# Kernel optimization log

Hardware: AMD Instinct MI355X
Metric: run time of the kernel (lower is better)

## Reference

```python
import jax, jax.numpy as jnp
import numpy as np

B, D, H, L, P, IMG = 8, 768, 12, 12, 16, 448
GRID = 28  # pos_embed grid (785 = 1 + 28*28)
EPS = 1e-5


def layer_norm(x, g, b):
    mu = jnp.mean(x, axis=-1, keepdims=True)
    var = jnp.mean((x - mu) ** 2, axis=-1, keepdims=True)
    return (x - mu) * jax.lax.rsqrt(var + EPS) * g + b


def setup_inputs() -> dict:
    key = jax.random.key(0)
    ks = jax.random.split(key, 12)
    s = 0.02
    inp = {
        "x": jax.random.normal(ks[0], (B, 3, IMG, IMG), dtype=jnp.float32),
        "conv_w": jax.random.normal(ks[1], (D, 3, P, P), dtype=jnp.float32) * s,
        "conv_b": jnp.zeros((D,), jnp.float32),
        "cls_token": jax.random.normal(ks[2], (1, 1, D), dtype=jnp.float32) * s,
        "pos_embed": jax.random.normal(ks[3], (1, 1 + GRID * GRID, D), dtype=jnp.float32) * s,
        "ln1_g": jnp.ones((L, D), jnp.float32),
        "ln1_b": jnp.zeros((L, D), jnp.float32),
        "qkv_w": jax.random.normal(ks[4], (L, D, 3 * D), dtype=jnp.float32) * s,
        "qkv_b": jnp.zeros((L, 3 * D), jnp.float32),
        "proj_w": jax.random.normal(ks[5], (L, D, D), dtype=jnp.float32) * s,
        "proj_b": jnp.zeros((L, D), jnp.float32),
        "ln2_g": jnp.ones((L, D), jnp.float32),
        "ln2_b": jnp.zeros((L, D), jnp.float32),
        "mlp_w1": jax.random.normal(ks[6], (L, D, 4 * D), dtype=jnp.float32) * s,
        "mlp_b1": jnp.zeros((L, 4 * D), jnp.float32),
        "mlp_w2": jax.random.normal(ks[7], (L, 4 * D, D), dtype=jnp.float32) * s,
        "mlp_b2": jnp.zeros((L, D), jnp.float32),
        "lnf_g": jnp.ones((D,), jnp.float32),
        "lnf_b": jnp.zeros((D,), jnp.float32),
    }
    return inp


def _vit_forward(x, conv_w, conv_b, cls_token, pos_embed,
                 ln1_g, ln1_b, qkv_w, qkv_b, proj_w, proj_b,
                 ln2_g, ln2_b, mlp_w1, mlp_b1, mlp_w2, mlp_b2, lnf_g, lnf_b):
    b = x.shape[0]
    # PatchEmbed: strided conv -> [B, D, 28, 28] -> [B, N, D]
    h = jax.lax.conv_general_dilated(
        x, conv_w, window_strides=(P, P), padding="VALID",
        dimension_numbers=("NCHW", "OIHW", "NCHW")) + conv_b[None, :, None, None]
    gh, gw = h.shape[2], h.shape[3]
    h = h.reshape(b, D, gh * gw).transpose(0, 2, 1)  # [B, N, D]
    # ClassEmbed
    h = jnp.concatenate([jnp.broadcast_to(cls_token, (b, 1, D)), h], axis=1)
    # PosEmbed with bicubic interpolation of the grid part (identity when gh=gw=28)
    grid = pos_embed[:, 1:, :].transpose(0, 2, 1).reshape(1, D, GRID, GRID)
    grid = jax.image.resize(grid, (1, D, gh, gw), method="bicubic")
    grid = grid.reshape(1, D, gh * gw).transpose(0, 2, 1)
    pos = jnp.concatenate([pos_embed[:, :1, :], grid], axis=1)
    h = h + pos

    scale = (D // H) ** (-0.5)

    def block(h, p):
        (l1g, l1b, qw, qb, pw, pb, l2g, l2b, w1, b1, w2, b2) = p
        y = layer_norm(h, l1g, l1b)
        m, n, d = y.shape
        qkv = (y @ qw + qb).reshape(m, n, 3, H, d // H)
        qkv = qkv.transpose(2, 0, 3, 1, 4)  # [3, B, H, N, dh]
        q, k, v = qkv[0], qkv[1], qkv[2]
        w = jax.nn.softmax(jnp.einsum("bhnd,bhmd->bhnm", q, k) * scale, axis=-1)
        attn = jnp.einsum("bhnm,bhmd->bhnd", w, v).transpose(0, 2, 1, 3).reshape(m, n, d)
        h = h + (attn @ pw + pb)
        y = layer_norm(h, l2g, l2b)
        h = h + (jax.nn.gelu(y @ w1 + b1, approximate=False) @ w2 + b2)
        return h, None

    params = (ln1_g, ln1_b, qkv_w, qkv_b, proj_w, proj_b,
              ln2_g, ln2_b, mlp_w1, mlp_b1, mlp_w2, mlp_b2)
    h, _ = jax.lax.scan(block, h, params)
    return layer_norm(h, lnf_g, lnf_b)[:, 0]


def reference(x, conv_w, conv_b, cls_token, pos_embed,
              ln1_g, ln1_b, qkv_w, qkv_b, proj_w, proj_b,
              ln2_g, ln2_b, mlp_w1, mlp_b1, mlp_w2, mlp_b2, lnf_g, lnf_b):
    return _vit_forward(x, conv_w, conv_b, cls_token, pos_embed,
                        ln1_g, ln1_b, qkv_w, qkv_b, proj_w, proj_b,
                        ln2_g, ln2_b, mlp_w1, mlp_b1, mlp_w2, mlp_b2, lnf_g, lnf_b)
```

## Files before the change

kernel.cpp:

```cpp
#include <hip/hip_runtime.h>
#include <math.h>

#define B_   8
#define D_   768
#define H_   12
#define L_   12
#define NTOK 785
#define NPAT 784
#define MTOT (B_ * NTOK)
#define MPAT (B_ * NPAT)
#define MPAD 6400
#define DFF  3072
#define EPS_ 1e-5f

typedef unsigned short u16;
typedef unsigned int   u32;
typedef short s16x8 __attribute__((ext_vector_type(8)));
typedef float f32x4 __attribute__((ext_vector_type(4)));

__device__ __forceinline__ u16 f2b(float f) {
    u32 u = __float_as_uint(f);
    u += 0x7fffu + ((u >> 16) & 1u);
    return (u16)(u >> 16);
}
__device__ __forceinline__ float b2f(u16 s) {
    return __uint_as_float(((u32)s) << 16);
}
__device__ __forceinline__ void gload_lds16(const void* g, void* l) {
    __builtin_amdgcn_global_load_lds(
        (const __attribute__((address_space(1))) void*)g,
        (__attribute__((address_space(3))) void*)l, 16, 0, 0);
}
__device__ __forceinline__ float gelu_exact(float x) {
    return 0.5f * x * (1.0f + erff(x * 0.70710678118654752f));
}

template <int MODE, int OUTBF>
__global__ __launch_bounds__(256) void mfma_gemm(
    const u16* __restrict__ A, const u16* __restrict__ WT,
    const float* __restrict__ bias, const float* __restrict__ R,
    void* __restrict__ Cout, int M, int N, int K)
{
    __shared__ u16 As[128 * 32];
    __shared__ u16 Bs[128 * 32];

    const int bm = blockIdx.y * 128;
    const int bn = blockIdx.x * 128;
    const int t  = threadIdx.x;
    const int wv = t >> 6, ln = t & 63;
    const int wr = wv >> 1, wc = wv & 1;

    f32x4 acc[4][4];
    const f32x4 z4 = {0.f, 0.f, 0.f, 0.f};
#pragma unroll
    for (int i = 0; i < 4; i++)
#pragma unroll
        for (int j = 0; j < 4; j++) acc[i][j] = z4;

    const int lrow = ln & 15;
    const int kq   = (ln >> 4) * 8;

    for (int kt = 0; kt < K; kt += 32) {
        __syncthreads();
#pragma unroll
        for (int g = 0; g < 2; g++) {
            const int c = wv * 64 + g * 256 + ln;
            const int r = c >> 2, kc = (c & 3) * 8;
            u16* ldsA = As + (wv * 64 + g * 256) * 8;
            u16* ldsB = Bs + (wv * 64 + g * 256) * 8;
            gload_lds16(A  + (size_t)(bm + r) * K + kt + kc, ldsA);
            gload_lds16(WT + (size_t)(bn + r) * K + kt + kc, ldsB);
        }
        __syncthreads();

        s16x8 af[4], bf[4];
#pragma unroll
        for (int i = 0; i < 4; i++)
            af[i] = *(const s16x8*)(As + (wr * 64 + i * 16 + lrow) * 32 + kq);
#pragma unroll
        for (int j = 0; j < 4; j++)
            bf[j] = *(const s16x8*)(Bs + (wc * 64 + j * 16 + lrow) * 32 + kq);
#pragma unroll
        for (int i = 0; i < 4; i++)
#pragma unroll
            for (int j = 0; j < 4; j++)
                acc[i][j] = __builtin_amdgcn_mfma_f32_16x16x32_bf16(
                    af[i], bf[j], acc[i][j], 0, 0, 0);
    }

    const int col_l = ln & 15;
    const int rq    = (ln >> 4) * 4;
#pragma unroll
    for (int j = 0; j < 4; j++) {
        const int col = bn + wc * 64 + j * 16 + col_l;
        const float bj = bias[col];
#pragma unroll
        for (int i = 0; i < 4; i++) {
            const int row0 = bm + wr * 64 + i * 16 + rq;
#pragma unroll
            for (int rg = 0; rg < 4; rg++) {
                const int row = row0 + rg;
                if (row >= M) continue;
                float v = acc[i][j][rg] + bj;
                if (MODE == 1) v = gelu_exact(v);
                if (MODE == 2) v += R[(size_t)row * N + col];
                if (OUTBF) ((u16*)Cout)[(size_t)row * N + col] = f2b(v);
                else       ((float*)Cout)[(size_t)row * N + col] = v;
            }
        }
    }
}

__global__ __launch_bounds__(256) void wt_kernel(
    const float* __restrict__ W, u16* __restrict__ WT, int K, int N)
{
    __shared__ float tile[32][33];
    const int n0 = blockIdx.x * 32, k0 = blockIdx.y * 32;
    const int r = threadIdx.x >> 3, c4 = (threadIdx.x & 7) * 4;
    const float4 v = *(const float4*)(W + (size_t)(k0 + r) * N + n0 + c4);
    tile[r][c4 + 0] = v.x; tile[r][c4 + 1] = v.y;
    tile[r][c4 + 2] = v.z; tile[r][c4 + 3] = v.w;
    __syncthreads();
    ushort4 o = make_ushort4(f2b(tile[c4 + 0][r]), f2b(tile[c4 + 1][r]),
                             f2b(tile[c4 + 2][r]), f2b(tile[c4 + 3][r]));
    *(ushort4*)(WT + (size_t)(n0 + r) * K + k0 + c4) = o;
}

__global__ __launch_bounds__(256) void flatcvt_kernel(
    const float* __restrict__ in, u16* __restrict__ out, int n4)
{
    const int i = blockIdx.x * 256 + threadIdx.x;
    if (i >= n4) return;
    const float4 v = ((const float4*)in)[i];
    ((ushort4*)out)[i] = make_ushort4(f2b(v.x), f2b(v.y), f2b(v.z), f2b(v.w));
}

__device__ __forceinline__ float block_sum(float s, float* red) {
#pragma unroll
    for (int off = 32; off; off >>= 1) s += __shfl_down(s, off, 64);
    const int wid = threadIdx.x >> 6;
    if ((threadIdx.x & 63) == 0) red[wid] = s;
    __syncthreads();
    if (threadIdx.x == 0) red[0] = red[0] + red[1] + red[2] + red[3];
    __syncthreads();
    const float r = red[0];
    __syncthreads();
    return r;
}

template <int OUTBF>
__global__ __launch_bounds__(256) void ln_kernel(
    const float* __restrict__ X, const float* __restrict__ g,
    const float* __restrict__ b, void* __restrict__ Y, size_t row_stride_in)
{
    __shared__ float red[4];
    const int row = blockIdx.x;
    const int t = threadIdx.x;
    const float* x = X + (size_t)row * row_stride_in;

    const float v0 = x[t], v1 = x[t + 256], v2 = x[t + 512];
    const float mean = block_sum(v0 + v1 + v2, red) * (1.0f / 768.0f);
    const float d0 = v0 - mean, d1 = v1 - mean, d2 = v2 - mean;
    const float var = block_sum(d0 * d0 + d1 * d1 + d2 * d2, red) * (1.0f / 768.0f);
    const float rs = rsqrtf(var + EPS_);

    const float o0 = d0 * rs * g[t] + b[t];
    const float o1 = d1 * rs * g[t + 256] + b[t + 256];
    const float o2 = d2 * rs * g[t + 512] + b[t + 512];
    if (OUTBF) {
        u16* y = (u16*)Y + (size_t)row * 768;
        y[t] = f2b(o0); y[t + 256] = f2b(o1); y[t + 512] = f2b(o2);
    } else {
        float* y = (float*)Y + (size_t)row * 768;
        y[t] = o0; y[t + 256] = o1; y[t + 512] = o2;
    }
}

#define AQB  128
#define AKT  64
#define KSTR 72

__global__ __launch_bounds__(256) void attn_kernel(
    const u16* __restrict__ qkv, u16* __restrict__ out)
{
    __shared__ u16 Ks[AKT * KSTR];
    __shared__ u16 Vt[64 * KSTR];
    __shared__ u16 Ps[4 * 32 * KSTR];

    const int bh = blockIdx.y;
    const int b  = bh / H_, hh = bh % H_;
    const int q0 = blockIdx.x * AQB;
    const int t  = threadIdx.x;
    const int w  = t >> 6, ln = t & 63;
    const int lrow = ln & 15, quad = ln >> 4;
    const size_t tokbase = (size_t)b * NTOK;

    s16x8 aq[2][2];
#pragma unroll
    for (int rowt = 0; rowt < 2; rowt++) {
        int qr = q0 + w * 32 + rowt * 16 + lrow;
        if (qr > NTOK - 1) qr = NTOK - 1;
        const u16* qp = qkv + (tokbase + qr) * 2304 + hh * 64 + quad * 8;
        aq[rowt][0] = *(const s16x8*)(qp);
        aq[rowt][1] = *(const s16x8*)(qp + 32);
    }

    f32x4 acc_o[2][4];
    const f32x4 z4 = {0.f, 0.f, 0.f, 0.f};
#pragma unroll
    for (int i = 0; i < 2; i++)
#pragma unroll
        for (int j = 0; j < 4; j++) acc_o[i][j] = z4;
    float m_r[2][4], l_r[2][4];
#pragma unroll
    for (int i = 0; i < 2; i++)
#pragma unroll
        for (int j = 0; j < 4; j++) { m_r[i][j] = -1e30f; l_r[i][j] = 0.f; }

    for (int j0 = 0; j0 < NTOK; j0 += AKT) {
        __syncthreads();
#pragma unroll
        for (int g = 0; g < 2; g++) {
            const int c = g * 256 + t;
            const int j = c >> 3, dc = c & 7;
            int jj = j0 + j; if (jj > NTOK - 1) jj = NTOK - 1;
            const s16x8 kv = *(const s16x8*)(
                qkv + (tokbase + jj) * 2304 + 768 + hh * 64 + dc * 8);
            *(s16x8*)(Ks + j * KSTR + dc * 8) = kv;
        }
#pragma unroll
        for (int g = 0; g < 2; g++) {
            const int c = g * 256 + t;
            const int j = c & 63, dc = c >> 6;
            int jj = j0 + j; if (jj > NTOK - 1) jj = NTOK - 1;
            const s16x8 vv = *(const s16x8*)(
                qkv + (tokbase + jj) * 2304 + 1536 + hh * 64 + dc * 8);
#pragma unroll
            for (int e = 0; e < 8; e++)
                Vt[(dc * 8 + e) * KSTR + j] = (u16)((const short*)&vv)[e];
        }
        __syncthreads();

        f32x4 acc_s[2][4];
#pragma unroll
        for (int i = 0; i < 2; i++)
#pragma unroll
            for (int j = 0; j < 4; j++) acc_s[i][j] = z4;
#pragma unroll
        for (int jt = 0; jt < 4; jt++) {
            const s16x8 bk0 =
                *(const s16x8*)(Ks + (jt * 16 + lrow) * KSTR + quad * 8);
            const s16x8 bk1 =
                *(const s16x8*)(Ks + (jt * 16 + lrow) * KSTR + 32 + quad * 8);
#pragma unroll
            for (int rowt = 0; rowt < 2; rowt++) {
                acc_s[rowt][jt] = __builtin_amdgcn_mfma_f32_16x16x32_bf16(
                    aq[rowt][0], bk0, acc_s[rowt][jt], 0, 0, 0);
                acc_s[rowt][jt] = __builtin_amdgcn_mfma_f32_16x16x32_bf16(
                    aq[rowt][1], bk1, acc_s[rowt][jt], 0, 0, 0);
            }
        }
        const f32x4 ninf = {-1e30f, -1e30f, -1e30f, -1e30f};
#pragma unroll
        for (int jt = 0; jt < 4; jt++) {
            const bool valid = (j0 + jt * 16 + lrow) < NTOK;
#pragma unroll
            for (int rowt = 0; rowt < 2; rowt++)
                acc_s[rowt][jt] = valid ? acc_s[rowt][jt] * 0.125f : ninf;
        }

#pragma unroll
        for (int rowt = 0; rowt < 2; rowt++) {
#pragma unroll
            for (int rg = 0; rg < 4; rg++) {
                float mx = fmaxf(fmaxf(acc_s[rowt][0][rg], acc_s[rowt][1][rg]),
                                 fmaxf(acc_s[rowt][2][rg], acc_s[rowt][3][rg]));
                mx = fmaxf(mx, __shfl_xor(mx, 1, 64));
                mx = fmaxf(mx, __shfl_xor(mx, 2, 64));
                mx = fmaxf(mx, __shfl_xor(mx, 4, 64));
                mx = fmaxf(mx, __shfl_xor(mx, 8, 64));
                const float nm = fmaxf(m_r[rowt][rg], mx);
                const float al = __expf(m_r[rowt][rg] - nm);
                m_r[rowt][rg] = nm;
                u16* prow = Ps + (size_t)(w * 32 + rowt * 16 + quad * 4 + rg) * KSTR
                            + lrow;
                float ps = 0.f;
#pragma unroll
                for (int jt = 0; jt < 4; jt++) {
                    const float p = __expf(acc_s[rowt][jt][rg] - nm);
                    ps += p;
                    prow[jt * 16] = f2b(p);
                }
                ps += __shfl_xor(ps, 1, 64);
                ps += __shfl_xor(ps, 2, 64);
                ps += __shfl_xor(ps, 4, 64);
                ps += __shfl_xor(ps, 8, 64);
                l_r[rowt][rg] = l_r[rowt][rg] * al + ps;
#pragma unroll
                for (int dt = 0; dt < 4; dt++) acc_o[rowt][dt][rg] *= al;
            }
        }

#pragma unroll
        for (int jc = 0; jc < 2; jc++) {
            const s16x8 ap0 = *(const s16x8*)(
                Ps + (w * 32 + lrow) * KSTR + jc * 32 + quad * 8);
            const s16x8 ap1 = *(const s16x8*)(
                Ps + (w * 32 + 16 + lrow) * KSTR + jc * 32 + quad * 8);
#pragma unroll
            for (int dt = 0; dt < 4; dt++) {
                const s16x8 bv = *(const s16x8*)(
                    Vt + (dt * 16 + lrow) * KSTR + jc * 32 + quad * 8);
                acc_o[0][dt] = __builtin_amdgcn_mfma_f32_16x16x32_bf16(
                    ap0, bv, acc_o[0][dt], 0, 0, 0);
                acc_o[1][dt] = __builtin_amdgcn_mfma_f32_16x16x32_bf16(
                    ap1, bv, acc_o[1][dt], 0, 0, 0);
            }
        }
    }

#pragma unroll
    for (int rowt = 0; rowt < 2; rowt++) {
#pragma unroll
        for (int rg = 0; rg < 4; rg++) {
            const int tok = q0 + w * 32 + rowt * 16 + quad * 4 + rg;
            if (tok >= NTOK) continue;
            const float inv = 1.0f / l_r[rowt][rg];
            u16* dst = out + (tokbase + tok) * D_ + hh * 64 + lrow;
#pragma unroll
            for (int dt = 0; dt < 4; dt++)
                dst[dt * 16] = f2b(acc_o[rowt][dt][rg] * inv);
        }
    }
}

__global__ __launch_bounds__(256) void im2col_kernel(
    const float* __restrict__ x, u16* __restrict__ patches)
{
    const int idx = blockIdx.x * 256 + threadIdx.x;
    if (idx >= MPAT * 96) return;
    const int prow = idx / 96;
    const int c8 = (idx % 96) * 8;
    const int bb = prow / NPAT;
    const int pp = prow % NPAT;
    const int gy = pp / 28, gx = pp % 28;
    const int c = c8 >> 8;
    const int rem = c8 & 255;
    const int py = rem >> 4, px = rem & 15;
    const float* src =
        x + (((size_t)(bb * 3 + c) * 448 + gy * 16 + py) * 448 + gx * 16 + px);
    const float4 a = *(const float4*)src;
    const float4 bq = *(const float4*)(src + 4);
    u16* dst = patches + (size_t)prow * 768 + c8;
    uint4 w4;
    w4.x = (u32)f2b(a.x) | ((u32)f2b(a.y) << 16);
    w4.y = (u32)f2b(a.z) | ((u32)f2b(a.w) << 16);
    w4.z = (u32)f2b(bq.x) | ((u32)f2b(bq.y) << 16);
    w4.w = (u32)f2b(bq.z) | ((u32)f2b(bq.w) << 16);
    *(uint4*)dst = w4;
}

__global__ __launch_bounds__(256) void assemble_kernel(
    const float* __restrict__ conv_out, const float* __restrict__ cls,
    const float* __restrict__ pos, float* __restrict__ h)
{
    const int idx = blockIdx.x * 256 + threadIdx.x;
    if (idx >= MTOT * 192) return;
    const int row = idx / 192;
    const int d = (idx % 192) * 4;
    const int bb = row / NTOK, n = row % NTOK;
    const float4 pv = *(const float4*)(pos + (size_t)n * 768 + d);
    float4 v;
    if (n == 0) {
        const float4 cv = *(const float4*)(cls + d);
        v = make_float4(cv.x + pv.x, cv.y + pv.y, cv.z + pv.z, cv.w + pv.w);
    } else {
        const float4 co =
            *(const float4*)(conv_out + (size_t)(bb * NPAT + n - 1) * 768 + d);
        v = make_float4(co.x + pv.x, co.y + pv.y, co.z + pv.z, co.w + pv.w);
    }
    *(float4*)(h + (size_t)row * 768 + d) = v;
}

extern "C" void kernel_launch(void* const* d_in, const int* in_sizes, int n_in,
                              void* d_out, int out_size, void* d_ws, size_t ws_size,
                              hipStream_t stream)
{
    const float* x      = (const float*)d_in[0];
    const float* conv_w = (const float*)d_in[1];
    const float* conv_b = (const float*)d_in[2];
    const float* cls    = (const float*)d_in[3];
    const float* pos    = (const float*)d_in[4];
    const float* ln1_g  = (const float*)d_in[5];
    const float* ln1_b  = (const float*)d_in[6];
    const float* qkv_w  = (const float*)d_in[7];
    const float* qkv_b  = (const float*)d_in[8];
    const float* proj_w = (const float*)d_in[9];
    const float* proj_b = (const float*)d_in[10];
    const float* ln2_g  = (const float*)d_in[11];
    const float* ln2_b  = (const float*)d_in[12];
    const float* w1     = (const float*)d_in[13];
    const float* b1     = (const float*)d_in[14];
    const float* w2     = (const float*)d_in[15];
    const float* b2     = (const float*)d_in[16];
    const float* lnf_g  = (const float*)d_in[17];
    const float* lnf_b  = (const float*)d_in[18];
    float* out = (float*)d_out;

    char* p = (char*)d_ws;
    auto alloc = [&](size_t bytes) {
        char* r = p;
        p += (bytes + 255) & ~(size_t)255;
        return r;
    };
    float* h    = (float*)alloc((size_t)MPAD * 768 * 4);
    u16*  y     = (u16*)alloc((size_t)MPAD * 768 * 2);
    u16*  qkv   = (u16*)alloc((size_t)MPAD * 2304 * 2);
    u16*  attn  = (u16*)alloc((size_t)MPAD * 768 * 2);
    u16*  mid   = (u16*)alloc((size_t)MPAD * 3072 * 2);
    u16*  wq    = (u16*)alloc((size_t)2304 * 768 * 2);
    u16*  wp    = (u16*)alloc((size_t)768 * 768 * 2);
    u16*  w1t   = (u16*)alloc((size_t)3072 * 768 * 2);
    u16*  w2t   = (u16*)alloc((size_t)768 * 3072 * 2);
    u16*  wcv   = (u16*)alloc((size_t)768 * 768 * 2);
    (void)alloc(4096);
    u16*   patches = mid;
    float* cbuf    = (float*)qkv;

    const dim3 blk(256);

    flatcvt_kernel<<<(768 * 768 / 4 + 255) / 256, blk, 0, stream>>>(conv_w, wcv,
                                                                    768 * 768 / 4);
    im2col_kernel<<<(MPAT * 96 + 255) / 256, blk, 0, stream>>>(x, patches);
    mfma_gemm<0, 0><<<dim3(6, MPAT / 128), blk, 0, stream>>>(
        patches, wcv, conv_b, nullptr, cbuf, MPAT, 768, 768);
    assemble_kernel<<<(MTOT * 192 + 255) / 256, blk, 0, stream>>>(cbuf, cls, pos, h);

    for (int l = 0; l < L_; l++) {
        wt_kernel<<<dim3(2304 / 32, 768 / 32), blk, 0, stream>>>(
            qkv_w + (size_t)l * 768 * 2304, wq, 768, 2304);
        wt_kernel<<<dim3(768 / 32, 768 / 32), blk, 0, stream>>>(
            proj_w + (size_t)l * 768 * 768, wp, 768, 768);
        wt_kernel<<<dim3(3072 / 32, 768 / 32), blk, 0, stream>>>(
            w1 + (size_t)l * 768 * 3072, w1t, 768, 3072);
        wt_kernel<<<dim3(768 / 32, 3072 / 32), blk, 0, stream>>>(
            w2 + (size_t)l * 3072 * 768, w2t, 3072, 768);

        ln_kernel<1><<<MTOT, blk, 0, stream>>>(h, ln1_g + l * 768, ln1_b + l * 768,
                                               y, 768);
        mfma_gemm<0, 1><<<dim3(18, 50), blk, 0, stream>>>(
            y, wq, qkv_b + l * 2304, nullptr, qkv, MTOT, 2304, 768);
        attn_kernel<<<dim3((NTOK + AQB - 1) / AQB, B_ * H_), blk, 0, stream>>>(
            qkv, attn);
        mfma_gemm<2, 0><<<dim3(6, 50), blk, 0, stream>>>(
            attn, wp, proj_b + l * 768, h, h, MTOT, 768, 768);
        ln_kernel<1><<<MTOT, blk, 0, stream>>>(h, ln2_g + l * 768, ln2_b + l * 768,
                                               y, 768);
        mfma_gemm<1, 1><<<dim3(24, 50), blk, 0, stream>>>(
            y, w1t, b1 + l * DFF, nullptr, mid, MTOT, DFF, 768);
        mfma_gemm<2, 0><<<dim3(6, 50), blk, 0, stream>>>(
            mid, w2t, b2 + l * 768, h, h, MTOT, 768, DFF);
    }

    ln_kernel<0><<<B_, blk, 0, stream>>>(h, lnf_g, lnf_b, out, (size_t)NTOK * 768);
}
```

Before: 4.816 ms.

## Use 64-row GEMM tiles for N=768 GEMMs and batch weight transposes

Templates the MFMA GEMM on the M tile size and uses 64-row tiles for the narrow N=768 GEMMs (projection, MLP down, patch embed), doubling the number of workgroups to better fill the GPU. When the workspace is large enough, all 12 layers' weights are transposed and converted to bf16 in four batched launches up front instead of 48 per-layer launches. The trade-offs are lower per-block reuse of B tiles and a larger workspace footprint.

After: 4.431 ms. -8.0%, faster.

```diff
diff --git a/kernel.cpp b/kernel.cpp
--- a/kernel.cpp
+++ b/kernel.cpp
@@ -35,25 +35,26 @@
     return 0.5f * x * (1.0f + erff(x * 0.70710678118654752f));
 }
 
-template <int MODE, int OUTBF>
+template <int BM, int MODE, int OUTBF>
 __global__ __launch_bounds__(256) void mfma_gemm(
     const u16* __restrict__ A, const u16* __restrict__ WT,
     const float* __restrict__ bias, const float* __restrict__ R,
     void* __restrict__ Cout, int M, int N, int K)
 {
-    __shared__ u16 As[128 * 32];
+    constexpr int MI = BM / 32;
+    __shared__ u16 As[BM * 32];
     __shared__ u16 Bs[128 * 32];
 
-    const int bm = blockIdx.y * 128;
+    const int bm = blockIdx.y * BM;
     const int bn = blockIdx.x * 128;
     const int t  = threadIdx.x;
     const int wv = t >> 6, ln = t & 63;
     const int wr = wv >> 1, wc = wv & 1;
 
-    f32x4 acc[4][4];
+    f32x4 acc[MI][4];
     const f32x4 z4 = {0.f, 0.f, 0.f, 0.f};
 #pragma unroll
-    for (int i = 0; i < 4; i++)
+    for (int i = 0; i < MI; i++)
 #pragma unroll
         for (int j = 0; j < 4; j++) acc[i][j] = z4;
 
@@ -63,25 +64,28 @@
     for (int kt = 0; kt < K; kt += 32) {
         __syncthreads();
 #pragma unroll
+        for (int g = 0; g < BM / 64; g++) {
+            const int c = g * 256 + wv * 64 + ln;
+            u16* ldsA = As + (g * 256 + wv * 64) * 8;
+            gload_lds16(A + (size_t)(bm + (c >> 2)) * K + kt + (c & 3) * 8, ldsA);
+        }
+#pragma unroll
         for (int g = 0; g < 2; g++) {
-            const int c = wv * 64 + g * 256 + ln;
-            const int r = c >> 2, kc = (c & 3) * 8;
-            u16* ldsA = As + (wv * 64 + g * 256) * 8;
-            u16* ldsB = Bs + (wv * 64 + g * 256) * 8;
-            gload_lds16(A  + (size_t)(bm + r) * K + kt + kc, ldsA);
-            gload_lds16(WT + (size_t)(bn + r) * K + kt + kc, ldsB);
+            const int c = g * 256 + wv * 64 + ln;
+            u16* ldsB = Bs + (g * 256 + wv * 64) * 8;
+            gload_lds16(WT + (size_t)(bn + (c >> 2)) * K + kt + (c & 3) * 8, ldsB);
         }
         __syncthreads();
 
-        s16x8 af[4], bf[4];
-#pragma unroll
-        for (int i = 0; i < 4; i++)
-            af[i] = *(const s16x8*)(As + (wr * 64 + i * 16 + lrow) * 32 + kq);
+        s16x8 af[MI], bf[4];
+#pragma unroll
+        for (int i = 0; i < MI; i++)
+            af[i] = *(const s16x8*)(As + (wr * (BM / 2) + i * 16 + lrow) * 32 + kq);
 #pragma unroll
         for (int j = 0; j < 4; j++)
             bf[j] = *(const s16x8*)(Bs + (wc * 64 + j * 16 + lrow) * 32 + kq);
 #pragma unroll
-        for (int i = 0; i < 4; i++)
+        for (int i = 0; i < MI; i++)
 #pragma unroll
             for (int j = 0; j < 4; j++)
                 acc[i][j] = __builtin_amdgcn_mfma_f32_16x16x32_bf16(
@@ -95,8 +99,8 @@
         const int col = bn + wc * 64 + j * 16 + col_l;
         const float bj = bias[col];
 #pragma unroll
-        for (int i = 0; i < 4; i++) {
-            const int row0 = bm + wr * 64 + i * 16 + rq;
+        for (int i = 0; i < MI; i++) {
+            const int row0 = bm + wr * (BM / 2) + i * 16 + rq;
 #pragma unroll
             for (int rg = 0; rg < 4; rg++) {
                 const int row = row0 + rg;
@@ -114,6 +118,9 @@
 __global__ __launch_bounds__(256) void wt_kernel(
     const float* __restrict__ W, u16* __restrict__ WT, int K, int N)
 {
+    const size_t lz = blockIdx.z;
+    W  += lz * (size_t)K * N;
+    WT += lz * (size_t)K * N;
     __shared__ float tile[32][33];
     const int n0 = blockIdx.x * 32, k0 = blockIdx.y * 32;
     const int r = threadIdx.x >> 3, c4 = (threadIdx.x & 7) * 4;
@@ -407,6 +414,18 @@
     const float* lnf_b  = (const float*)d_in[18];
     float* out = (float*)d_out;
 
+    auto al = [](size_t v) { return (v + 255) & ~(size_t)255; };
+
+    const size_t base_need =
+        al((size_t)MPAD * 768 * 4) + al((size_t)MPAD * 768 * 2) +
+        al((size_t)MPAD * 2304 * 2) + al((size_t)MPAD * 768 * 2) +
+        al((size_t)MPAD * 3072 * 2) + al((size_t)768 * 768 * 2) + 4096;
+    const size_t per_layer_w =
+        al((size_t)2304 * 768 * 2) + al((size_t)768 * 768 * 2) +
+        al((size_t)3072 * 768 * 2) + al((size_t)768 * 3072 * 2);
+    const bool batched = ws_size >= base_need + 12 * per_layer_w;
+    const int LW = batched ? 12 : 1;
+
     char* p = (char*)d_ws;
     auto alloc = [&](size_t bytes) {
         char* r = p;
@@ -418,10 +437,10 @@
     u16*  qkv   = (u16*)alloc((size_t)MPAD * 2304 * 2);
     u16*  attn  = (u16*)alloc((size_t)MPAD * 768 * 2);
     u16*  mid   = (u16*)alloc((size_t)MPAD * 3072 * 2);
-    u16*  wq    = (u16*)alloc((size_t)2304 * 768 * 2);
-    u16*  wp    = (u16*)alloc((size_t)768 * 768 * 2);
-    u16*  w1t   = (u16*)alloc((size_t)3072 * 768 * 2);
-    u16*  w2t   = (u16*)alloc((size_t)768 * 3072 * 2);
+    u16*  wq    = (u16*)alloc((size_t)LW * 2304 * 768 * 2);
+    u16*  wp    = (u16*)alloc((size_t)LW * 768 * 768 * 2);
+    u16*  w1t   = (u16*)alloc((size_t)LW * 3072 * 768 * 2);
+    u16*  w2t   = (u16*)alloc((size_t)LW * 768 * 3072 * 2);
     u16*  wcv   = (u16*)alloc((size_t)768 * 768 * 2);
     (void)alloc(4096);
     u16*   patches = mid;
@@ -432,34 +451,53 @@
     flatcvt_kernel<<<(768 * 768 / 4 + 255) / 256, blk, 0, stream>>>(conv_w, wcv,
                                                                     768 * 768 / 4);
     im2col_kernel<<<(MPAT * 96 + 255) / 256, blk, 0, stream>>>(x, patches);
-    mfma_gemm<0, 0><<<dim3(6, MPAT / 128), blk, 0, stream>>>(
+    mfma_gemm<64, 0, 0><<<dim3(6, MPAT / 64), blk, 0, stream>>>(
         patches, wcv, conv_b, nullptr, cbuf, MPAT, 768, 768);
     assemble_kernel<<<(MTOT * 192 + 255) / 256, blk, 0, stream>>>(cbuf, cls, pos, h);
 
+    if (batched) {
+        wt_kernel<<<dim3(2304 / 32, 768 / 32, 12), blk, 0, stream>>>(
+            qkv_w, wq, 768, 2304);
+        wt_kernel<<<dim3(768 / 32, 768 / 32, 12), blk, 0, stream>>>(
+            proj_w, wp, 768, 768);
+        wt_kernel<<<dim3(3072 / 32, 768 / 32, 12), blk, 0, stream>>>(
+            w1, w1t, 768, 3072);
+        wt_kernel<<<dim3(768 / 32, 3072 / 32, 12), blk, 0, stream>>>(
+            w2, w2t, 3072, 768);
+    }
+
+    const int my64 = (MTOT + 63) / 64;
+
     for (int l = 0; l < L_; l++) {
-        wt_kernel<<<dim3(2304 / 32, 768 / 32), blk, 0, stream>>>(
-            qkv_w + (size_t)l * 768 * 2304, wq, 768, 2304);
-        wt_kernel<<<dim3(768 / 32, 768 / 32), blk, 0, stream>>>(
-            proj_w + (size_t)l * 768 * 768, wp, 768, 768);
-        wt_kernel<<<dim3(3072 / 32, 768 / 32), blk, 0, stream>>>(
-            w1 + (size_t)l * 768 * 3072, w1t, 768, 3072);
-        wt_kernel<<<dim3(768 / 32, 3072 / 32), blk, 0, stream>>>(
-            w2 + (size_t)l * 3072 * 768, w2t, 3072, 768);
+        u16* wq_l  = wq  + (size_t)(batched ? l : 0) * 2304 * 768;
+        u16* wp_l  = wp  + (size_t)(batched ? l : 0) * 768 * 768;
+        u16* w1t_l = w1t + (size_t)(batched ? l : 0) * 3072 * 768;
+        u16* w2t_l = w2t + (size_t)(batched ? l : 0) * 768 * 3072;
+        if (!batched) {
+            wt_kernel<<<dim3(2304 / 32, 768 / 32), blk, 0, stream>>>(
+                qkv_w + (size_t)l * 768 * 2304, wq_l, 768, 2304);
+            wt_kernel<<<dim3(768 / 32, 768 / 32), blk, 0, stream>>>(
+                proj_w + (size_t)l * 768 * 768, wp_l, 768, 768);
+            wt_kernel<<<dim3(3072 / 32, 768 / 32), blk, 0, stream>>>(
+                w1 + (size_t)l * 768 * 3072, w1t_l, 768, 3072);
+            wt_kernel<<<dim3(768 / 32, 3072 / 32), blk, 0, stream>>>(
+                w2 + (size_t)l * 3072 * 768, w2t_l, 3072, 768);
+        }
 
         ln_kernel<1><<<MTOT, blk, 0, stream>>>(h, ln1_g + l * 768, ln1_b + l * 768,
                                                y, 768);
-        mfma_gemm<0, 1><<<dim3(18, 50), blk, 0, stream>>>(
-            y, wq, qkv_b + l * 2304, nullptr, qkv, MTOT, 2304, 768);
+        mfma_gemm<128, 0, 1><<<dim3(18, 50), blk, 0, stream>>>(
+            y, wq_l, qkv_b + l * 2304, nullptr, qkv, MTOT, 2304, 768);
         attn_kernel<<<dim3((NTOK + AQB - 1) / AQB, B_ * H_), blk, 0, stream>>>(
             qkv, attn);
-        mfma_gemm<2, 0><<<dim3(6, 50), blk, 0, stream>>>(
-            attn, wp, proj_b + l * 768, h, h, MTOT, 768, 768);
+        mfma_gemm<64, 2, 0><<<dim3(6, my64), blk, 0, stream>>>(
+            attn, wp_l, proj_b + l * 768, h, h, MTOT, 768, 768);
         ln_kernel<1><<<MTOT, blk, 0, stream>>>(h, ln2_g + l * 768, ln2_b + l * 768,
                                                y, 768);
-        mfma_gemm<1, 1><<<dim3(24, 50), blk, 0, stream>>>(
-            y, w1t, b1 + l * DFF, nullptr, mid, MTOT, DFF, 768);
-        mfma_gemm<2, 0><<<dim3(6, 50), blk, 0, stream>>>(
-            mid, w2t, b2 + l * 768, h, h, MTOT, 768, DFF);
+        mfma_gemm<128, 1, 1><<<dim3(24, 50), blk, 0, stream>>>(
+            y, w1t_l, b1 + l * DFF, nullptr, mid, MTOT, DFF, 768);
+        mfma_gemm<64, 2, 0><<<dim3(6, my64), blk, 0, stream>>>(
+            mid, w2t_l, b2 + l * 768, h, h, MTOT, 768, DFF);
     }
 
     ln_kernel<0><<<B_, blk, 0, stream>>>(h, lnf_g, lnf_b, out, (size_t)NTOK * 768);
```
